# Kernel optimization log

Hardware: AMD Instinct MI355X
Metric: run time of the kernel (lower is better)

Reference implementation:

```python
import jax, jax.numpy as jnp
import numpy as np

NUM_CONCAT = 3

def setup_inputs() -> dict:
    key = jax.random.key(0)
    k1, k2, k3 = jax.random.split(key, 3)
    x = jax.random.normal(k1, (4, 2048, 4096), dtype=jnp.float32)
    W = jax.random.normal(k2, (12288, 4096), dtype=jnp.float32) * 0.02
    b = jax.random.normal(k3, (12288,), dtype=jnp.float32) * 0.02
    return {"x": x, "W": W, "b": b}

def reference(x, W, b):
    # Fused concat-linear: one GEMM over the concatenated weight, then split.
    # x: [B, S, D]; W: [NUM_CONCAT*H, D]; b: [NUM_CONCAT*H]
    y = jnp.einsum('bsd,od->bso', x, W) + b  # [B, S, NUM_CONCAT*H]
    hidden = y.shape[-1] // NUM_CONCAT
    return tuple(y[..., i * hidden:(i + 1) * hidden] for i in range(NUM_CONCAT))
```

## Files before the change

kernel.cpp:

```cpp
#include <hip/hip_runtime.h>
#include <stdint.h>


typedef __attribute__((ext_vector_type(8))) short short8;
typedef __attribute__((ext_vector_type(4))) float f32x4;

#define BM  256
#define BN  256
#define BKT 64

__device__ __forceinline__ unsigned short f2bf(float f) {
  union { float f; unsigned u; } v; v.f = f;
  unsigned u = v.u;
  u += 0x7FFFu + ((u >> 16) & 1u);
  return (unsigned short)(u >> 16);
}

__global__ void cast2_f32_to_bf16(const float* __restrict__ inA,
                                  unsigned short* __restrict__ outA, long long nA8,
                                  const float* __restrict__ inB,
                                  unsigned short* __restrict__ outB, long long nB8) {
  long long i = (long long)blockIdx.x * blockDim.x + threadIdx.x;
  const float* in; unsigned short* out; long long k;
  if (i < nA8) { in = inA; out = outA; k = i; }
  else {
    k = i - nA8;
    if (k >= nB8) return;
    in = inB; out = outB;
  }
  const float4* p = (const float4*)in;
  float4 a = p[2 * k + 0];
  float4 b = p[2 * k + 1];
  uint4 o;
  o.x = (unsigned)f2bf(a.x) | ((unsigned)f2bf(a.y) << 16);
  o.y = (unsigned)f2bf(a.z) | ((unsigned)f2bf(a.w) << 16);
  o.z = (unsigned)f2bf(b.x) | ((unsigned)f2bf(b.y) << 16);
  o.w = (unsigned)f2bf(b.z) | ((unsigned)f2bf(b.w) << 16);
  ((uint4*)out)[k] = o;
}

__device__ __forceinline__ void gload16(const unsigned short* src, short* dst) {
  __builtin_amdgcn_global_load_lds(
      (const __attribute__((address_space(1))) unsigned int*)src,
      (__attribute__((address_space(3))) unsigned int*)dst, 16, 0, 0);
}

__global__ __launch_bounds__(512, 2)
void gemm256_bias_split(const unsigned short* __restrict__ A,
                        const unsigned short* __restrict__ B,
                        const float* __restrict__ bias,
                        float* __restrict__ out,
                        int M, int N, int K, int H) {
  __shared__ short sA[2][BM * BKT];
  __shared__ short sB[2][BN * BKT];

  const int tid  = threadIdx.x;
  const int lane = tid & 63;
  const int r16  = lane & 15;
  const int q    = lane >> 4;
  const int wave = tid >> 6;
  const int wr   = wave >> 2;
  const int wc   = wave & 3;
  const int AR   = wr * 128;
  const int BR   = wc * 64;

  const int ntx = N / BN;
  const int nwg = gridDim.x;
  const int mty = nwg / ntx;
  int bid = blockIdx.x;
  int m0, n0;
  if ((nwg & 7) == 0 && (mty & 7) == 0) {
    const int GM  = mty >> 3;
    const int xcd = bid & 7;
    const int l   = bid >> 3;
    const int lm  = l % GM;
    const int ln  = l / GM;
    m0 = (xcd * GM + lm) * BM;
    n0 = ln * BN;
  } else if ((nwg & 7) == 0) {
    const int cpx = nwg >> 3;
    const int b2  = (bid & 7) * cpx + (bid >> 3);
    n0 = (b2 % ntx) * BN;
    m0 = (b2 / ntx) * BM;
  } else {
    n0 = (bid % ntx) * BN;
    m0 = (bid / ntx) * BM;
  }

  const int NT = K / BKT;

  const int c   = tid & 7;
  const int pr  = tid >> 3;
  const int csz = c ^ (pr & 7);
  const unsigned short* gA = A + (size_t)(m0 + pr) * K + csz * 8;
  const int prB = (pr & 31) + ((tid >> 8) << 6);
  const unsigned short* gB = B + (size_t)(n0 + prB) * K + csz * 8;
  const int dA = pr * 64 + c * 8;
  const int dB = prB * 64 + c * 8;
  const size_t K128 = (size_t)128 * K;

  auto stageA = [&](int buf, int kt, int u) {
    const unsigned short* s = gA + (size_t)(u * 64) * K + kt * BKT;
    short* d = &sA[buf][dA + u * 4096];
    gload16(s, d);
    gload16(s + K128, d + 8192);
  };
  auto stageB = [&](int buf, int kt, int u) {
    const unsigned short* s = gB + (size_t)(u * 32) * K + kt * BKT;
    short* d = &sB[buf][dB + u * 2048];
    gload16(s, d);
    gload16(s + K128, d + 8192);
  };

  const int swz  = r16 & 7;
  const int aoff = (AR + r16) * 64;
  const int boff = (BR + r16) * 64;
  const int ck0  = (q ^ swz) * 8;
  const int ck1  = ((4 + q) ^ swz) * 8;

  f32x4 acc[8][4];
#pragma unroll
  for (int i = 0; i < 8; ++i)
#pragma unroll
    for (int j = 0; j < 4; ++j) acc[i][j] = (f32x4){0.f, 0.f, 0.f, 0.f};

  stageA(0, 0, 0); stageB(0, 0, 0); stageA(0, 0, 1); stageB(0, 0, 1);
  stageA(1, 1, 0); stageB(1, 1, 0); stageA(1, 1, 1);
  asm volatile("s_waitcnt vmcnt(6)" ::: "memory");
  __builtin_amdgcn_s_barrier();

  short8 alo[4][2], ahi[4][2], b01[2][2], b23[2][2];

  for (int j = 0; j < NT; ++j) {
    const int P = j & 1;
    const short* bA = sA[P];
    const short* bB = sB[P];

#pragma unroll
    for (int mf = 0; mf < 4; ++mf) {
      alo[mf][0] = *(const short8*)&bA[aoff + mf * 1024 + ck0];
      alo[mf][1] = *(const short8*)&bA[aoff + mf * 1024 + ck1];
    }
#pragma unroll
    for (int nf = 0; nf < 2; ++nf) {
      b01[nf][0] = *(const short8*)&bB[boff + nf * 1024 + ck0];
      b01[nf][1] = *(const short8*)&bB[boff + nf * 1024 + ck1];
    }
    if (j + 1 < NT) stageB(P ^ 1, j + 1, 1);
    __builtin_amdgcn_s_barrier();
    asm volatile("s_waitcnt lgkmcnt(0)" ::: "memory");
    __builtin_amdgcn_sched_barrier(0);
    __builtin_amdgcn_s_setprio(1);
#pragma unroll
    for (int mf = 0; mf < 4; ++mf)
#pragma unroll
      for (int nf = 0; nf < 2; ++nf) {
        acc[mf][nf] = __builtin_amdgcn_mfma_f32_16x16x32_bf16(alo[mf][0], b01[nf][0], acc[mf][nf], 0, 0, 0);
        acc[mf][nf] = __builtin_amdgcn_mfma_f32_16x16x32_bf16(alo[mf][1], b01[nf][1], acc[mf][nf], 0, 0, 0);
      }
    __builtin_amdgcn_s_setprio(0);
    __builtin_amdgcn_s_barrier();

#pragma unroll
    for (int nf = 0; nf < 2; ++nf) {
      b23[nf][0] = *(const short8*)&bB[boff + (nf + 2) * 1024 + ck0];
      b23[nf][1] = *(const short8*)&bB[boff + (nf + 2) * 1024 + ck1];
    }
    if (j + 2 < NT) stageA(P, j + 2, 0);
    __builtin_amdgcn_s_barrier();
    asm volatile("s_waitcnt lgkmcnt(0)" ::: "memory");
    __builtin_amdgcn_sched_barrier(0);
    __builtin_amdgcn_s_setprio(1);
#pragma unroll
    for (int mf = 0; mf < 4; ++mf)
#pragma unroll
      for (int nf = 0; nf < 2; ++nf) {
        acc[mf][nf + 2] = __builtin_amdgcn_mfma_f32_16x16x32_bf16(alo[mf][0], b23[nf][0], acc[mf][nf + 2], 0, 0, 0);
        acc[mf][nf + 2] = __builtin_amdgcn_mfma_f32_16x16x32_bf16(alo[mf][1], b23[nf][1], acc[mf][nf + 2], 0, 0, 0);
      }
    __builtin_amdgcn_s_setprio(0);
    __builtin_amdgcn_s_barrier();

#pragma unroll
    for (int mf = 0; mf < 4; ++mf) {
      ahi[mf][0] = *(const short8*)&bA[aoff + (mf + 4) * 1024 + ck0];
      ahi[mf][1] = *(const short8*)&bA[aoff + (mf + 4) * 1024 + ck1];
    }
    if (j + 2 < NT) stageB(P, j + 2, 0);
    __builtin_amdgcn_s_barrier();
    asm volatile("s_waitcnt lgkmcnt(0)" ::: "memory");
    __builtin_amdgcn_sched_barrier(0);
    __builtin_amdgcn_s_setprio(1);
#pragma unroll
    for (int mf = 0; mf < 4; ++mf)
#pragma unroll
      for (int nf = 0; nf < 2; ++nf) {
        acc[mf + 4][nf + 2] = __builtin_amdgcn_mfma_f32_16x16x32_bf16(ahi[mf][0], b23[nf][0], acc[mf + 4][nf + 2], 0, 0, 0);
        acc[mf + 4][nf + 2] = __builtin_amdgcn_mfma_f32_16x16x32_bf16(ahi[mf][1], b23[nf][1], acc[mf + 4][nf + 2], 0, 0, 0);
      }
    __builtin_amdgcn_s_setprio(0);
    __builtin_amdgcn_s_barrier();

    if (j + 2 < NT) stageA(P, j + 2, 1);
    __builtin_amdgcn_s_barrier();
    __builtin_amdgcn_s_setprio(1);
#pragma unroll
    for (int mf = 0; mf < 4; ++mf)
#pragma unroll
      for (int nf = 0; nf < 2; ++nf) {
        acc[mf + 4][nf] = __builtin_amdgcn_mfma_f32_16x16x32_bf16(ahi[mf][0], b01[nf][0], acc[mf + 4][nf], 0, 0, 0);
        acc[mf + 4][nf] = __builtin_amdgcn_mfma_f32_16x16x32_bf16(ahi[mf][1], b01[nf][1], acc[mf + 4][nf], 0, 0, 0);
      }
    __builtin_amdgcn_s_setprio(0);
    if (j < NT - 2) asm volatile("s_waitcnt vmcnt(6)" ::: "memory");
    else            asm volatile("s_waitcnt vmcnt(0)" ::: "memory");
    __builtin_amdgcn_s_barrier();
  }

  float bj[4];
#pragma unroll
  for (int nf = 0; nf < 4; ++nf) bj[nf] = bias[n0 + BR + nf * 16 + r16];
  const size_t chunk_elems = (size_t)M * H;
#pragma unroll
  for (int nf = 0; nf < 4; ++nf) {
    const int n  = n0 + BR + nf * 16 + r16;
    const int ci = n / H;
    const int h  = n - ci * H;
    float* obase = out + (size_t)ci * chunk_elems + h;
#pragma unroll
    for (int mf = 0; mf < 8; ++mf) {
      const int mb = m0 + AR + mf * 16 + q * 4;
#pragma unroll
      for (int rr = 0; rr < 4; ++rr) {
        obase[(size_t)(mb + rr) * H] = acc[mf][nf][rr] + bj[nf];
      }
    }
  }
}

#define FTILE 128
#define FBK   64

__global__ __launch_bounds__(256)
void gemm_bias_split_fb(const float* __restrict__ Af32,
                        const float* __restrict__ Bf32,
                        const float* __restrict__ bias,
                        float* __restrict__ out,
                        int M, int N, int K, int H) {
  __shared__ short sA[FTILE * FBK];
  __shared__ short sB[FTILE * FBK];

  const int tid  = threadIdx.x;
  const int lane = tid & 63;
  const int r16  = lane & 15;
  const int q    = lane >> 4;
  const int wave = tid >> 6;
  const int wm   = (wave & 1) * 64;
  const int wn   = (wave >> 1) * 64;
  const int m0   = blockIdx.y * FTILE;
  const int n0   = blockIdx.x * FTILE;

  f32x4 acc[4][4];
#pragma unroll
  for (int i = 0; i < 4; ++i)
#pragma unroll
    for (int j = 0; j < 4; ++j)
      acc[i][j] = (f32x4){0.f, 0.f, 0.f, 0.f};

  for (int k0 = 0; k0 < K; k0 += FBK) {
    __syncthreads();
#pragma unroll
    for (int it = 0; it < 4; ++it) {
      const int chunk = it * 256 + tid;
      const int row   = chunk >> 3;
      const int c     = chunk & 7;
      const int cs    = c ^ (row & 7);
      const float* gA = Af32 + (size_t)(m0 + row) * K + (k0 + cs * 8);
      const float* gB = Bf32 + (size_t)(n0 + row) * K + (k0 + cs * 8);
      float4 a0 = ((const float4*)gA)[0], a1 = ((const float4*)gA)[1];
      float4 b0 = ((const float4*)gB)[0], b1 = ((const float4*)gB)[1];
      short8 va, vb;
      va[0] = (short)f2bf(a0.x); va[1] = (short)f2bf(a0.y);
      va[2] = (short)f2bf(a0.z); va[3] = (short)f2bf(a0.w);
      va[4] = (short)f2bf(a1.x); va[5] = (short)f2bf(a1.y);
      va[6] = (short)f2bf(a1.z); va[7] = (short)f2bf(a1.w);
      vb[0] = (short)f2bf(b0.x); vb[1] = (short)f2bf(b0.y);
      vb[2] = (short)f2bf(b0.z); vb[3] = (short)f2bf(b0.w);
      vb[4] = (short)f2bf(b1.x); vb[5] = (short)f2bf(b1.y);
      vb[6] = (short)f2bf(b1.z); vb[7] = (short)f2bf(b1.w);
      *(short8*)&sA[chunk * 8] = va;
      *(short8*)&sB[chunk * 8] = vb;
    }
    __syncthreads();

#pragma unroll
    for (int ks = 0; ks < 2; ++ks) {
      short8 af[4], bfr[4];
#pragma unroll
      for (int i = 0; i < 4; ++i) {
        const int row = wm + i * 16 + r16;
        const int cc  = ks * 4 + q;
        af[i] = *(const short8*)&sA[row * FBK + (cc ^ (row & 7)) * 8];
      }
#pragma unroll
      for (int j = 0; j < 4; ++j) {
        const int row = wn + j * 16 + r16;
        const int cc  = ks * 4 + q;
        bfr[j] = *(const short8*)&sB[row * FBK + (cc ^ (row & 7)) * 8];
      }
#pragma unroll
      for (int i = 0; i < 4; ++i)
#pragma unroll
        for (int j = 0; j < 4; ++j)
          acc[i][j] = __builtin_amdgcn_mfma_f32_16x16x32_bf16(
              af[i], bfr[j], acc[i][j], 0, 0, 0);
    }
  }

  float bj[4];
#pragma unroll
  for (int j = 0; j < 4; ++j) bj[j] = bias[n0 + wn + j * 16 + r16];
  const size_t chunk_elems = (size_t)M * H;
#pragma unroll
  for (int j = 0; j < 4; ++j) {
    const int n  = n0 + wn + j * 16 + r16;
    const int ci = n / H;
    const int h  = n - ci * H;
    float* obase = out + (size_t)ci * chunk_elems + h;
#pragma unroll
    for (int i = 0; i < 4; ++i) {
      const int mb = m0 + wm + i * 16 + q * 4;
#pragma unroll
      for (int rr = 0; rr < 4; ++rr) {
        obase[(size_t)(mb + rr) * H] = acc[i][j][rr] + bj[j];
      }
    }
  }
}

extern "C" void kernel_launch(void* const* d_in, const int* in_sizes, int n_in,
                              void* d_out, int out_size, void* d_ws, size_t ws_size,
                              hipStream_t stream) {
  const float* x = (const float*)d_in[0];
  const float* W = (const float*)d_in[1];
  const float* b = (const float*)d_in[2];
  float* out = (float*)d_out;

  const int N = in_sizes[2];
  const int K = in_sizes[1] / N;
  const int M = in_sizes[0] / K;
  const int H = N / 3;

  const size_t nA = (size_t)M * K;
  const size_t nB = (size_t)N * K;
  const bool ws_ok = ws_size >= (nA + nB) * sizeof(unsigned short);
  const bool big   = ws_ok && (M % BM == 0) && (N % BN == 0) &&
                     (K % BKT == 0) && (K / BKT >= 4);

  if (big) {
    unsigned short* xa = (unsigned short*)d_ws;
    unsigned short* wb = xa + nA;
    const long long nA8 = (long long)(nA / 8);
    const long long nB8 = (long long)(nB / 8);
    const long long tot = nA8 + nB8;
    cast2_f32_to_bf16<<<(int)((tot + 255) / 256), 256, 0, stream>>>(
        x, xa, nA8, W, wb, nB8);
    const int nblocks = (M / BM) * (N / BN);
    gemm256_bias_split<<<nblocks, 512, 0, stream>>>(xa, wb, b, out, M, N, K, H);
  } else {
    dim3 grid(N / FTILE, M / FTILE);
    gemm_bias_split_fb<<<grid, 256, 0, stream>>>(x, W, b, out, M, N, K, H);
  }
}
```

Measured before the change: 1.405 ms.

## Stage GEMM epilogue through LDS for coalesced float4 stores; grid-stride cast kernel

The GEMM epilogue now writes bias-added accumulators into a per-wave LDS tile, reusing the operand shared memory as one flat array. It then reads the tile back row-wise and issues coalesced float4 global stores, replacing scattered 4-byte column-strided stores. The cast kernel becomes a grid-stride loop over float4 elements with a fixed grid of 2048 blocks. A guard requiring H divisible by 64 keeps each wave's 64-column strip inside one output chunk. The added LDS round trip and waits lengthen the epilogue, and the cast kernel now stores 8 bytes per thread instead of 16.

After: 1.245 ms. 11.4% less time.

```diff
diff --git a/kernel.cpp b/kernel.cpp
--- a/kernel.cpp
+++ b/kernel.cpp
@@ -16,27 +16,27 @@
   return (unsigned short)(u >> 16);
 }
 
-__global__ void cast2_f32_to_bf16(const float* __restrict__ inA,
-                                  unsigned short* __restrict__ outA, long long nA8,
-                                  const float* __restrict__ inB,
-                                  unsigned short* __restrict__ outB, long long nB8) {
-  long long i = (long long)blockIdx.x * blockDim.x + threadIdx.x;
-  const float* in; unsigned short* out; long long k;
-  if (i < nA8) { in = inA; out = outA; k = i; }
-  else {
-    k = i - nA8;
-    if (k >= nB8) return;
-    in = inB; out = outB;
-  }
-  const float4* p = (const float4*)in;
-  float4 a = p[2 * k + 0];
-  float4 b = p[2 * k + 1];
-  uint4 o;
-  o.x = (unsigned)f2bf(a.x) | ((unsigned)f2bf(a.y) << 16);
-  o.y = (unsigned)f2bf(a.z) | ((unsigned)f2bf(a.w) << 16);
-  o.z = (unsigned)f2bf(b.x) | ((unsigned)f2bf(b.y) << 16);
-  o.w = (unsigned)f2bf(b.z) | ((unsigned)f2bf(b.w) << 16);
-  ((uint4*)out)[k] = o;
+__global__ __launch_bounds__(256)
+void cast_all_f32_to_bf16(const float* __restrict__ a, unsigned long long na4,
+                          unsigned short* __restrict__ oa,
+                          const float* __restrict__ b, unsigned long long nb4,
+                          unsigned short* __restrict__ ob) {
+  const unsigned long long stride = (unsigned long long)gridDim.x * blockDim.x;
+  const unsigned long long i0 = (unsigned long long)blockIdx.x * blockDim.x + threadIdx.x;
+  for (unsigned long long k = i0; k < na4; k += stride) {
+    float4 v = ((const float4*)a)[k];
+    uint2 o;
+    o.x = (unsigned)f2bf(v.x) | ((unsigned)f2bf(v.y) << 16);
+    o.y = (unsigned)f2bf(v.z) | ((unsigned)f2bf(v.w) << 16);
+    ((uint2*)oa)[k] = o;
+  }
+  for (unsigned long long k = i0; k < nb4; k += stride) {
+    float4 v = ((const float4*)b)[k];
+    uint2 o;
+    o.x = (unsigned)f2bf(v.x) | ((unsigned)f2bf(v.y) << 16);
+    o.y = (unsigned)f2bf(v.z) | ((unsigned)f2bf(v.w) << 16);
+    ((uint2*)ob)[k] = o;
+  }
 }
 
 __device__ __forceinline__ void gload16(const unsigned short* src, short* dst) {
@@ -51,8 +51,9 @@
                         const float* __restrict__ bias,
                         float* __restrict__ out,
                         int M, int N, int K, int H) {
-  __shared__ short sA[2][BM * BKT];
-  __shared__ short sB[2][BN * BKT];
+  __shared__ short smem[2 * BM * BKT + 2 * BN * BKT];
+  short* const sA0 = smem;
+  short* const sB0 = smem + 2 * BM * BKT;
 
   const int tid  = threadIdx.x;
   const int lane = tid & 63;
@@ -101,13 +102,13 @@
 
   auto stageA = [&](int buf, int kt, int u) {
     const unsigned short* s = gA + (size_t)(u * 64) * K + kt * BKT;
-    short* d = &sA[buf][dA + u * 4096];
+    short* d = sA0 + buf * (BM * BKT) + dA + u * 4096;
     gload16(s, d);
     gload16(s + K128, d + 8192);
   };
   auto stageB = [&](int buf, int kt, int u) {
     const unsigned short* s = gB + (size_t)(u * 32) * K + kt * BKT;
-    short* d = &sB[buf][dB + u * 2048];
+    short* d = sB0 + buf * (BN * BKT) + dB + u * 2048;
     gload16(s, d);
     gload16(s + K128, d + 8192);
   };
@@ -133,8 +134,8 @@
 
   for (int j = 0; j < NT; ++j) {
     const int P = j & 1;
-    const short* bA = sA[P];
-    const short* bB = sB[P];
+    const short* bA = sA0 + P * (BM * BKT);
+    const short* bB = sB0 + P * (BN * BKT);
 
 #pragma unroll
     for (int mf = 0; mf < 4; ++mf) {
@@ -220,21 +221,31 @@
   float bj[4];
 #pragma unroll
   for (int nf = 0; nf < 4; ++nf) bj[nf] = bias[n0 + BR + nf * 16 + r16];
-  const size_t chunk_elems = (size_t)M * H;
-#pragma unroll
-  for (int nf = 0; nf < 4; ++nf) {
-    const int n  = n0 + BR + nf * 16 + r16;
-    const int ci = n / H;
-    const int h  = n - ci * H;
-    float* obase = out + (size_t)ci * chunk_elems + h;
-#pragma unroll
-    for (int mf = 0; mf < 8; ++mf) {
-      const int mb = m0 + AR + mf * 16 + q * 4;
-#pragma unroll
-      for (int rr = 0; rr < 4; ++rr) {
-        obase[(size_t)(mb + rr) * H] = acc[mf][nf][rr] + bj[nf];
-      }
-    }
+  const int nb = n0 + BR;
+  const int ci = nb / H;
+  const int h0 = nb - ci * H;
+  float* const obase = out + (size_t)ci * ((size_t)M * H) + h0;
+  const int mbase = m0 + AR;
+  float* const T = reinterpret_cast<float*>(smem) + wave * 4096;
+
+#pragma unroll
+  for (int p = 0; p < 2; ++p) {
+#pragma unroll
+    for (int mf = 0; mf < 4; ++mf)
+#pragma unroll
+      for (int nf = 0; nf < 4; ++nf)
+#pragma unroll
+        for (int rr = 0; rr < 4; ++rr)
+          T[(mf * 16 + q * 4 + rr) * 64 + nf * 16 + r16] =
+              acc[p * 4 + mf][nf][rr] + bj[nf];
+    asm volatile("s_waitcnt lgkmcnt(0)" ::: "memory");
+#pragma unroll
+    for (int i = 0; i < 16; ++i) {
+      const int row = i * 4 + q;
+      float4 v = *(const float4*)&T[row * 64 + r16 * 4];
+      *(float4*)&obase[(size_t)(mbase + p * 64 + row) * H + r16 * 4] = v;
+    }
+    asm volatile("s_waitcnt lgkmcnt(0)" ::: "memory");
   }
 }
 
@@ -355,16 +366,14 @@
   const size_t nB = (size_t)N * K;
   const bool ws_ok = ws_size >= (nA + nB) * sizeof(unsigned short);
   const bool big   = ws_ok && (M % BM == 0) && (N % BN == 0) &&
-                     (K % BKT == 0) && (K / BKT >= 4);
+                     (K % BKT == 0) && (K / BKT >= 4) && ((H & 63) == 0);
 
   if (big) {
     unsigned short* xa = (unsigned short*)d_ws;
     unsigned short* wb = xa + nA;
-    const long long nA8 = (long long)(nA / 8);
-    const long long nB8 = (long long)(nB / 8);
-    const long long tot = nA8 + nB8;
-    cast2_f32_to_bf16<<<(int)((tot + 255) / 256), 256, 0, stream>>>(
-        x, xa, nA8, W, wb, nB8);
+    cast_all_f32_to_bf16<<<2048, 256, 0, stream>>>(
+        x, (unsigned long long)(nA / 4), xa,
+        W, (unsigned long long)(nB / 4), wb);
     const int nblocks = (M / BM) * (N / BN);
     gemm256_bias_split<<<nblocks, 512, 0, stream>>>(xa, wb, b, out, M, N, K, H);
   } else {
```
